# Kernel optimization log

Measured on AMD Instinct MI355X. Metric: run time of the kernel, lower is better.

Reference implementation:

```python
import jax, jax.numpy as jnp
import numpy as np

N, E = 10000, 160000
IN_C, HID, OUT_C = 128, 128, 64
LAYERS, HEADS = 3, 8
D_HEAD = HID // HEADS


def setup_inputs() -> dict:
    key = jax.random.key(0)
    ks = jax.random.split(key, 12)
    sc = lambda k, shape, fan: (jax.random.normal(k, shape, jnp.float32) / np.float32(np.sqrt(fan)))
    return dict(
        x=jax.random.normal(ks[0], (N, IN_C), jnp.float32),
        edge_index=jax.random.randint(ks[1], (2, E), 0, N, jnp.int32),
        W1=sc(ks[2], (IN_C, HID), IN_C), b1=jnp.zeros((HID,), jnp.float32),
        Wq=sc(ks[3], (LAYERS, HID, HID), HID), bq=jnp.zeros((LAYERS, HID), jnp.float32),
        Wk=sc(ks[4], (LAYERS, HID, HID), HID), bk=jnp.zeros((LAYERS, HID), jnp.float32),
        Wv=sc(ks[5], (LAYERS, HID, HID), HID), bv=jnp.zeros((LAYERS, HID), jnp.float32),
        W2=sc(ks[6], (HID, OUT_C), HID), b2=jnp.zeros((OUT_C,), jnp.float32),
    )


def reference(x, edge_index, W1, b1, Wq, bq, Wk, bk, Wv, bv, W2, b2):
    n = x.shape[0]
    # gcn_norm with self-loops (edge weights = 1)
    loops = jnp.arange(n, dtype=edge_index.dtype)
    src = jnp.concatenate([edge_index[0], loops])  # x_j source nodes
    dst = jnp.concatenate([edge_index[1], loops])  # x_i target nodes (aggregation)
    deg = jax.ops.segment_sum(jnp.ones_like(src, dtype=x.dtype), dst, num_segments=n)
    dinv = jnp.where(deg > 0, jax.lax.rsqrt(deg), jnp.zeros_like(deg))
    norm = dinv[src] * dinv[dst]  # [E+N]

    # dropout layers are identity in eval mode
    h = jax.nn.relu(x @ W1 + b1)
    x_all = h[:, None, :]  # [N, 1, C]

    scale = np.float32(1.0 / np.sqrt(D_HEAD))
    for l in range(LAYERS):
        L = x_all.shape[1]
        # project at node level (linear commutes with gather)
        q = (x_all[:, -1] @ Wq[l] + bq[l])[dst]              # [Et, C], query = last-layer target feats
        k = (x_all @ Wk[l] + bk[l])[src]                     # [Et, L, C], key = source history
        v = (x_all @ Wv[l] + bv[l])[src]                     # [Et, L, C]
        Et = q.shape[0]
        qh = q.reshape(Et, HEADS, D_HEAD)
        kh = k.reshape(Et, L, HEADS, D_HEAD)
        vh = v.reshape(Et, L, HEADS, D_HEAD)
        scores = jnp.einsum('ehd,elhd->ehl', qh, kh) * scale  # attention over history axis L
        attn = jax.nn.softmax(scores, axis=-1)                 # (attn dropout is identity in eval)
        msg = jnp.einsum('ehl,elhd->ehd', attn, vh).reshape(Et, HID)
        agg = jax.ops.segment_sum(norm[:, None] * msg, dst, num_segments=n)
        h_new = jax.nn.relu(agg)
        x_all = jnp.concatenate([x_all, h_new[:, None, :]], axis=1)

    logits = x_all[:, -1] @ W2 + b2
    return jax.nn.log_softmax(logits, axis=1)
```

## Files before the change

kernel.cpp:

```cpp
#include <hip/hip_runtime.h>
#include <hip/hip_fp16.h>
#include <math.h>

#define NN 10000
#define EE 160000
#define HID 128
constexpr int N128 = NN * HID;
constexpr int PSTR = 768;
constexpr int HOFF = 384;

typedef _Float16 f16;
typedef f16 half8 __attribute__((ext_vector_type(8)));
typedef f16 f16x2 __attribute__((ext_vector_type(2)));
typedef float f32x4 __attribute__((ext_vector_type(4)));

#if __has_builtin(__builtin_amdgcn_fdot2)
__device__ inline float fdot2(f16x2 a, f16x2 b, float c) { return __builtin_amdgcn_fdot2(a, b, c, false); }
#else
__device__ inline float fdot2(f16x2 a, f16x2 b, float c) {
    return fmaf((float)a[0], (float)b[0], fmaf((float)a[1], (float)b[1], c));
}
#endif

__global__ __launch_bounds__(256) void zero_ws(int4* __restrict__ p) {
    p[blockIdx.x * 256 + threadIdx.x] = make_int4(0, 0, 0, 0);
}

__global__ __launch_bounds__(256) void cnt_count(const int* __restrict__ dst, int* __restrict__ cnt) {
    int e = blockIdx.x * 256 + threadIdx.x;
    if (e < EE) atomicAdd(&cnt[dst[e]], 1);
}

__global__ __launch_bounds__(256) void scan_rowptr(const int* __restrict__ cnt, int* __restrict__ rowptr,
                                                   float* __restrict__ dinv) {
    __shared__ int part[256];
    const int PER = (NN + 255) / 256;
    int t = threadIdx.x;
    int base = t * PER;
    int sum = 0;
    for (int i = 0; i < PER; ++i) {
        int idx = base + i;
        if (idx < NN) {
            int c = cnt[idx];
            sum += c;
            dinv[idx] = rsqrtf((float)c + 1.0f);
        }
    }
    part[t] = sum;
    __syncthreads();
    for (int ofs = 1; ofs < 256; ofs <<= 1) {
        int v = (t >= ofs) ? part[t - ofs] : 0;
        __syncthreads();
        part[t] += v;
        __syncthreads();
    }
    int run = (t > 0) ? part[t - 1] : 0;
    for (int i = 0; i < PER; ++i) {
        int idx = base + i;
        if (idx <= NN) rowptr[idx] = run;
        if (idx < NN) run += cnt[idx];
    }
}

__global__ __launch_bounds__(256) void scatter_edges(const int* __restrict__ ei,
                                                     const int* __restrict__ rowptr,
                                                     int* __restrict__ fill,
                                                     int* __restrict__ esorted) {
    int e = blockIdx.x * 256 + threadIdx.x;
    if (e < EE) {
        int s = ei[e], d = ei[EE + e];
        int pos = rowptr[d] + atomicAdd(&fill[d], 1);
        esorted[pos] = s;
    }
}

__global__ __launch_bounds__(256) void wprep(const float* __restrict__ W1, const float* __restrict__ Wq,
                                             const float* __restrict__ Wk, const float* __restrict__ Wv,
                                             const float* __restrict__ W2, f16* __restrict__ Wt) {
    int b = blockIdx.x;
    f16* dst = Wt + (size_t)b * 16384;
    int t = threadIdx.x;
    if (b == 10) {
        int oc = t & 63, k0 = (t >> 6) * 32;
        for (int kk = 0; kk < 32; ++kk) {
            int k = k0 + kk;
            dst[oc * 128 + k] = (f16)W2[(size_t)k * 64 + oc];
        }
        return;
    }
    const float* src = (b == 0) ? W1
                     : (b < 4)  ? Wq + (size_t)(b - 1) * 16384
                     : (b < 7)  ? Wk + (size_t)(b - 4) * 16384
                                : Wv + (size_t)(b - 7) * 16384;
    int oc = t >> 1;
    int k0 = (t & 1) * 64;
    for (int kk = 0; kk < 64; ++kk) {
        int k = k0 + kk;
        dst[oc * 128 + k] = (f16)src[k * 128 + oc];
    }
}

struct GJob {
    const void* in; const f16* Wt; const float* bias; const float* rowscale;
    void* out; int ldi; int ldo; int mode; int inF32;
    const f16* Wt2; const float* bias2;
};
struct GJobs { GJob j[7]; };

__global__ __launch_bounds__(256) void gemm_mfma(GJobs jobs, int nrows) {
    const GJob jb = jobs.j[blockIdx.y];
    __shared__ f16 Xl[64 * 128];
    __shared__ f16 Wl[128 * 128];
    const int t = threadIdx.x;
    const int row0 = blockIdx.x * 64;

    half8 zero8;
#pragma unroll
    for (int z = 0; z < 8; ++z) zero8[z] = (f16)0.f;

#pragma unroll
    for (int it = 0; it < 4; ++it) {
        int idx = t + it * 256;
        int r = idx >> 4, c = idx & 15;
        int gr = row0 + r;
        half8 v = zero8;
        if (gr < nrows) {
            if (jb.inF32) {
                const float* fin = (const float*)jb.in + (size_t)gr * jb.ldi + c * 8;
                float4 f0 = ((const float4*)fin)[0];
                float4 f1 = ((const float4*)fin)[1];
                v[0] = (f16)f0.x; v[1] = (f16)f0.y; v[2] = (f16)f0.z; v[3] = (f16)f0.w;
                v[4] = (f16)f1.x; v[5] = (f16)f1.y; v[6] = (f16)f1.z; v[7] = (f16)f1.w;
            } else {
                v = *(const half8*)((const f16*)jb.in + (size_t)gr * jb.ldi + c * 8);
            }
        }
        *(half8*)((char*)Xl + r * 256 + ((c * 16) ^ ((r & 7) << 4))) = v;
    }
#pragma unroll
    for (int it = 0; it < 8; ++it) {
        int idx = t + it * 256;
        int r = idx >> 4, c = idx & 15;
        half8 v = *(const half8*)(jb.Wt + (size_t)r * 128 + c * 8);
        *(half8*)((char*)Wl + r * 256 + ((c * 16) ^ ((r & 7) << 4))) = v;
    }
    __syncthreads();

    const int w = t >> 6, l = t & 63;
    const int lr = l & 15;
    const int lk = l >> 4;

    f32x4 acc[8];
#pragma unroll
    for (int tn = 0; tn < 8; ++tn)
#pragma unroll
        for (int i = 0; i < 4; ++i) acc[tn][i] = 0.f;

    const int arow = w * 16 + lr;
    const int axor = (arow & 7) << 4;
    const int bxor = (lr & 7) << 4;

#pragma unroll
    for (int ks = 0; ks < 4; ++ks) {
        int koff = (ks * 4 + lk) * 16;
        half8 a = *(const half8*)((const char*)Xl + arow * 256 + (koff ^ axor));
#pragma unroll
        for (int tn = 0; tn < 8; ++tn) {
            int oc = tn * 16 + lr;
            half8 b = *(const half8*)((const char*)Wl + oc * 256 + (koff ^ bxor));
            acc[tn] = __builtin_amdgcn_mfma_f32_16x16x32_f16(a, b, acc[tn], 0, 0, 0);
        }
    }

    const int rbase = row0 + w * 16 + (lk << 2);
    float brs[4];
#pragma unroll
    for (int i = 0; i < 4; ++i)
        brs[i] = jb.rowscale ? ((rbase + i < nrows) ? jb.rowscale[rbase + i] : 0.f) : 1.0f;
    float bsv[8];
#pragma unroll
    for (int tn = 0; tn < 8; ++tn) bsv[tn] = jb.bias[tn * 16 + lr];

    if (jb.mode == 0) {
        float* op = (float*)jb.out;
#pragma unroll
        for (int tn = 0; tn < 8; ++tn)
#pragma unroll
            for (int i = 0; i < 4; ++i) {
                int gr = rbase + i;
                if (gr < nrows) op[(size_t)gr * jb.ldo + tn * 16 + lr] = acc[tn][i] + brs[i] * bsv[tn];
            }
    } else if (jb.mode == 1) {
        f16* op = (f16*)jb.out;
#pragma unroll
        for (int tn = 0; tn < 8; ++tn)
#pragma unroll
            for (int i = 0; i < 4; ++i) {
                int gr = rbase + i;
                if (gr < nrows) op[(size_t)gr * jb.ldo + tn * 16 + lr] = (f16)fmaxf(acc[tn][i] + brs[i] * bsv[tn], 0.f);
            }
    } else if (jb.mode == 2) {
        f16* op = (f16*)jb.out;
#pragma unroll
        for (int tn = 0; tn < 8; ++tn)
#pragma unroll
            for (int i = 0; i < 4; ++i) {
                int gr = rbase + i;
                if (gr < nrows) op[(size_t)gr * jb.ldo + tn * 16 + lr] = (f16)(acc[tn][i] + brs[i] * bsv[tn]);
            }
    } else {
        __syncthreads();
#pragma unroll
        for (int tn = 0; tn < 8; ++tn)
#pragma unroll
            for (int i = 0; i < 4; ++i) {
                f16 v = (f16)fmaxf(acc[tn][i] + brs[i] * bsv[tn], 0.f);
                int lrow = w * 16 + (lk << 2) + i;
                int col = tn * 16 + lr;
                int byte = lrow * 256 + ((((col >> 3) * 16) ^ ((lrow & 7) << 4))) + (col & 7) * 2;
                *(f16*)((char*)Xl + byte) = v;
            }
#pragma unroll
        for (int it = 0; it < 4; ++it) {
            int idx = t + it * 256;
            int r = idx >> 4, c = idx & 15;
            half8 v = *(const half8*)(jb.Wt2 + (size_t)r * 128 + c * 8);
            *(half8*)((char*)Wl + r * 256 + ((c * 16) ^ ((r & 7) << 4))) = v;
        }
        __syncthreads();

        f32x4 acc2[4];
#pragma unroll
        for (int tn = 0; tn < 4; ++tn)
#pragma unroll
            for (int i = 0; i < 4; ++i) acc2[tn][i] = 0.f;
#pragma unroll
        for (int ks = 0; ks < 4; ++ks) {
            int koff = (ks * 4 + lk) * 16;
            half8 a = *(const half8*)((const char*)Xl + arow * 256 + (koff ^ axor));
#pragma unroll
            for (int tn = 0; tn < 4; ++tn) {
                int oc = tn * 16 + lr;
                half8 b = *(const half8*)((const char*)Wl + oc * 256 + (koff ^ bxor));
                acc2[tn] = __builtin_amdgcn_mfma_f32_16x16x32_f16(a, b, acc2[tn], 0, 0, 0);
            }
        }
        float bs2[4];
#pragma unroll
        for (int tn = 0; tn < 4; ++tn) bs2[tn] = jb.bias2[tn * 16 + lr];
#pragma unroll
        for (int i = 0; i < 4; ++i) {
            float lg[4];
#pragma unroll
            for (int tn = 0; tn < 4; ++tn) lg[tn] = acc2[tn][i] + bs2[tn];
            float m = fmaxf(fmaxf(lg[0], lg[1]), fmaxf(lg[2], lg[3]));
#pragma unroll
            for (int sft = 1; sft <= 8; sft <<= 1) m = fmaxf(m, __shfl_xor(m, sft));
            float den = 0.f;
#pragma unroll
            for (int tn = 0; tn < 4; ++tn) den += __expf(lg[tn] - m);
#pragma unroll
            for (int sft = 1; sft <= 8; sft <<= 1) den += __shfl_xor(den, sft);
            float lden = logf(den);
            int gr = rbase + i;
            if (gr < nrows) {
                float* op = (float*)jb.out + (size_t)gr * jb.ldo;
#pragma unroll
                for (int tn = 0; tn < 4; ++tn) op[tn * 16 + lr] = lg[tn] - m - lden;
            }
        }
    }
}

__global__ __launch_bounds__(256) void sgather4(
    const int* __restrict__ rowptr, const int* __restrict__ esorted,
    const float* __restrict__ dinv,
    const f16* __restrict__ hsrc , f16* __restrict__ Sh, float* __restrict__ srow) {
    int d = (blockIdx.x * 256 + threadIdx.x) >> 6;
    int lane = threadIdx.x & 63;
    if (d >= NN) return;
    int i0 = rowptr[d], i1 = rowptr[d + 1];
    int nE = i1 - i0 + 1;
    float dvd = dinv[d];
    float ax = 0.f, ay = 0.f, ssum = 0.f;

    auto ld_idx = [&](int jb, int (&s)[4], float (&dv)[4]) {
#pragma unroll
        for (int u = 0; u < 4; ++u) {
            int j = jb + u;
            int ss = (j < nE - 1) ? esorted[i0 + j] : d;
            s[u] = ss;
            dv[u] = (j < nE) ? dinv[ss] : 0.f;
        }
    };
    auto ld_dat = [&](const int (&s)[4], f16x2 (&hh)[4]) {
#pragma unroll
        for (int u = 0; u < 4; ++u)
            hh[u] = *(const f16x2*)(hsrc + (size_t)s[u] * PSTR + lane * 2);
    };
    auto comp = [&](const float (&dv)[4], const f16x2 (&hh)[4]) {
#pragma unroll
        for (int u = 0; u < 4; ++u) {
            ax = fmaf(dv[u], (float)hh[u][0], ax);
            ay = fmaf(dv[u], (float)hh[u][1], ay);
            ssum += dv[u];
        }
    };

    int sA[4], sB[4], sC[4], sD[4];
    float wA[4], wB[4], wC[4], wD[4];
    f16x2 hA[4], hB[4];
    ld_idx(0, sA, wA); ld_dat(sA, hA);
    ld_idx(4, sB, wB);
    for (int base = 0; base < nE; base += 8) {
        ld_idx(base + 8, sC, wC);
        ld_dat(sB, hB);
        comp(wA, hA);
        ld_idx(base + 12, sD, wD);
        ld_dat(sC, hA);
        comp(wB, hB);
#pragma unroll
        for (int u = 0; u < 4; ++u) { wA[u] = wC[u]; sB[u] = sD[u]; wB[u] = wD[u]; }
    }
    f16x2 o; o[0] = (f16)(dvd * ax); o[1] = (f16)(dvd * ay);
    *(f16x2*)(Sh + (size_t)d * 128 + lane * 2) = o;
    if (lane == 0) srow[d] = dvd * ssum;
}

template<int L>
__global__ __launch_bounds__(256) void node_attn4(
    const int* __restrict__ rowptr, const int* __restrict__ esorted,
    const float* __restrict__ dinv,
    const f16* __restrict__ qh, const f16* __restrict__ pack,
    f16* __restrict__ uh) {
    int d = (blockIdx.x * 256 + threadIdx.x) >> 6;
    int lane = threadIdx.x & 63;
    if (d >= NN) return;
    int i0 = rowptr[d], i1 = rowptr[d + 1];
    int nE = i1 - i0 + 1;
    float dvd = dinv[d];
    f16x2 q2 = *(const f16x2*)(qh + (size_t)d * 128 + lane * 2);
    float ax = 0.f, ay = 0.f;

    auto ld_idx = [&](int jb, int (&s)[4], float (&dv)[4]) {
#pragma unroll
        for (int u = 0; u < 4; ++u) {
            int j = jb + u;
            int ss = (j < nE - 1) ? esorted[i0 + j] : d;
            s[u] = ss;
            dv[u] = (j < nE) ? dinv[ss] : 0.f;
        }
    };
    auto ld_dat = [&](const int (&s)[4], f16x2 (&k2)[4][L], f16x2 (&hh)[4][L]) {
#pragma unroll
        for (int u = 0; u < 4; ++u) {
            const f16* bp = pack + (size_t)s[u] * PSTR + lane * 2;
#pragma unroll
            for (int l = 0; l < L; ++l) {
                k2[u][l] = *(const f16x2*)(bp + l * 128);
                hh[u][l] = *(const f16x2*)(bp + HOFF + l * 128);
            }
        }
    };
    auto comp = [&](const float (&dv)[4], const f16x2 (&k2)[4][L], const f16x2 (&hh)[4][L]) {
#pragma unroll
        for (int u = 0; u < 4; ++u) {
            float sc[L];
#pragma unroll
            for (int l = 0; l < L; ++l) {
                float p = fdot2(q2, k2[u][l], 0.f);
                p += __shfl_xor(p, 1);
                p += __shfl_xor(p, 2);
                p += __shfl_xor(p, 4);
                sc[l] = p * 0.25f;
            }
            float m = sc[0];
#pragma unroll
            for (int l = 1; l < L; ++l) m = fmaxf(m, sc[l]);
            float den = 0.f;
#pragma unroll
            for (int l = 0; l < L; ++l) { sc[l] = __expf(sc[l] - m); den += sc[l]; }
            float wgt = dv[u] * __builtin_amdgcn_rcpf(den);
#pragma unroll
            for (int l = 0; l < L; ++l) {
                float wl = sc[l] * wgt;
                ax = fmaf(wl, (float)hh[u][l][0], ax);
                ay = fmaf(wl, (float)hh[u][l][1], ay);
            }
        }
    };

    int sA[4], sB[4], sC[4], sD[4];
    float wA[4], wB[4], wC[4], wD[4];
    f16x2 kA[4][L], hA[4][L], kB[4][L], hB[4][L];
    ld_idx(0, sA, wA); ld_dat(sA, kA, hA);
    ld_idx(4, sB, wB);
    for (int base = 0; base < nE; base += 8) {
        ld_idx(base + 8, sC, wC);
        ld_dat(sB, kB, hB);
        comp(wA, kA, hA);
        ld_idx(base + 12, sD, wD);
        ld_dat(sC, kA, hA);
        comp(wB, kB, hB);
#pragma unroll
        for (int u = 0; u < 4; ++u) { wA[u] = wC[u]; sB[u] = sD[u]; wB[u] = wD[u]; }
    }
    f16x2 o; o[0] = (f16)(dvd * ax); o[1] = (f16)(dvd * ay);
    *(f16x2*)(uh + (size_t)d * 128 + lane * 2) = o;
}

extern "C" void kernel_launch(void* const* d_in, const int* in_sizes, int n_in,
                              void* d_out, int out_size, void* d_ws, size_t ws_size,
                              hipStream_t stream) {
    (void)in_sizes; (void)n_in; (void)out_size; (void)ws_size;
    const float* x  = (const float*)d_in[0];
    const int*   ei = (const int*)d_in[1];
    const float* W1 = (const float*)d_in[2];
    const float* b1 = (const float*)d_in[3];
    const float* Wq = (const float*)d_in[4];
    const float* bq = (const float*)d_in[5];
    const float* Wk = (const float*)d_in[6];
    const float* bk = (const float*)d_in[7];
    const float* Wv = (const float*)d_in[8];
    const float* bv = (const float*)d_in[9];
    const float* W2 = (const float*)d_in[10];
    const float* b2 = (const float*)d_in[11];
    float* out = (float*)d_out;

    int*    cnt     = (int*)d_ws;
    int*    fill    = cnt + 16384;
    int*    rowptr  = fill + 16384;
    int*    esorted = rowptr + 16384;
    float*  dinv    = (float*)(esorted + 163840);
    float*  srow    = dinv + 16384;
    f16*    pack    = (f16*)(srow + 16384);
    f16*    Sh      = pack + (size_t)NN * PSTR;
    f16*    qh      = Sh + N128;
    f16*    uh      = qh + N128;
    f16*    Wt      = uh + N128;

    zero_ws<<<32, 256, 0, stream>>>((int4*)cnt);
    cnt_count<<<(EE + 255) / 256, 256, 0, stream>>>(ei + EE, cnt);
    scan_rowptr<<<1, 256, 0, stream>>>(cnt, rowptr, dinv);
    scatter_edges<<<(EE + 255) / 256, 256, 0, stream>>>(ei, rowptr, fill, esorted);
    wprep<<<11, 256, 0, stream>>>(W1, Wq, Wk, Wv, W2, Wt);

    const int gx = (NN + 63) / 64;
    auto WT = [&](int m) { return Wt + (size_t)m * 16384; };
    auto H  = [&](int lev) { return pack + HOFF + lev * 128; };
    auto K  = [&](int lev) { return pack + lev * 128; };

    {
        GJobs jobs{};
        jobs.j[0] = {x, WT(0), b1, nullptr, H(0), HID, PSTR, 1, 1, nullptr, nullptr};
        gemm_mfma<<<dim3(gx, 1), 256, 0, stream>>>(jobs, NN);
    }

    const int nblocks = (NN * 64 + 255) / 256;

    sgather4<<<nblocks, 256, 0, stream>>>(rowptr, esorted, dinv, pack + HOFF, Sh, srow);
    {
        GJobs jobs{};
        jobs.j[0] = {Sh, WT(7), bv, srow, H(1), HID, PSTR, 1, 0, nullptr, nullptr};
        gemm_mfma<<<dim3(gx, 1), 256, 0, stream>>>(jobs, NN);
    }

    for (int l = 1; l < 3; ++l) {
        int L = l + 1;
        GJobs jobs{};
        jobs.j[0] = {H(L - 1), WT(1 + l), bq + l * HID, nullptr, qh, PSTR, HID, 2, 0, nullptr, nullptr};
        for (int lev = 0; lev < L; ++lev)
            jobs.j[1 + lev] = {H(lev), WT(4 + l), bk + l * HID, nullptr, K(lev), PSTR, PSTR, 2, 0, nullptr, nullptr};
        gemm_mfma<<<dim3(gx, 1 + L), 256, 0, stream>>>(jobs, NN);

        if (L == 2) node_attn4<2><<<nblocks, 256, 0, stream>>>(rowptr, esorted, dinv, qh, pack, uh);
        if (L == 3) node_attn4<3><<<nblocks, 256, 0, stream>>>(rowptr, esorted, dinv, qh, pack, uh);

        GJobs vjob{};
        if (L == 2) {
            vjob.j[0] = {uh, WT(7 + l), bv + l * HID, srow, H(2), HID, PSTR, 1, 0, nullptr, nullptr};
        } else {
            vjob.j[0] = {uh, WT(7 + l), bv + l * HID, srow, out, HID, 64, 3, 0, WT(10), b2};
        }
        gemm_mfma<<<dim3(gx, 1), 256, 0, stream>>>(vjob, NN);
    }
}
```

Before: 206.1 us.

## Split wave into four edge groups with 16-byte half8 loads in gather kernels

The gather and attention kernels are restructured so each 64-lane wave processes four edges at once, with every 16-lane quarter loading a 16-byte half8 slice of the 128-wide row rather than each lane loading 4 bytes. Per-lane accumulators are then reduced across quarters with cross-lane shuffles. The per-head dot-product reduction needs one shuffle instead of three. The zeroing kernel is folded into the weight-prep kernel to save a launch. This aims to raise memory-level parallelism and cut load instruction count, at the cost of more registers per lane and a final cross-quarter reduction.

```diff
diff --git a/kernel.cpp b/kernel.cpp
--- a/kernel.cpp
+++ b/kernel.cpp
@@ -21,10 +21,6 @@
     return fmaf((float)a[0], (float)b[0], fmaf((float)a[1], (float)b[1], c));
 }
 #endif
-
-__global__ __launch_bounds__(256) void zero_ws(int4* __restrict__ p) {
-    p[blockIdx.x * 256 + threadIdx.x] = make_int4(0, 0, 0, 0);
-}
 
 __global__ __launch_bounds__(256) void cnt_count(const int* __restrict__ dst, int* __restrict__ cnt) {
     int e = blockIdx.x * 256 + threadIdx.x;
@@ -74,12 +70,17 @@
     }
 }
 
-__global__ __launch_bounds__(256) void wprep(const float* __restrict__ W1, const float* __restrict__ Wq,
-                                             const float* __restrict__ Wk, const float* __restrict__ Wv,
-                                             const float* __restrict__ W2, f16* __restrict__ Wt) {
+__global__ __launch_bounds__(256) void prep_fused(const float* __restrict__ W1, const float* __restrict__ Wq,
+                                                  const float* __restrict__ Wk, const float* __restrict__ Wv,
+                                                  const float* __restrict__ W2, f16* __restrict__ Wt,
+                                                  int4* __restrict__ zbuf) {
     int b = blockIdx.x;
+    int t = threadIdx.x;
+    if (b >= 11) {
+        zbuf[(b - 11) * 256 + t] = make_int4(0, 0, 0, 0);
+        return;
+    }
     f16* dst = Wt + (size_t)b * 16384;
-    int t = threadIdx.x;
     if (b == 10) {
         int oc = t & 63, k0 = (t >> 6) * 32;
         for (int kk = 0; kk < 32; ++kk) {
@@ -272,141 +273,131 @@
     }
 }
 
-__global__ __launch_bounds__(256) void sgather4(
+__global__ __launch_bounds__(256) void sgather5(
     const int* __restrict__ rowptr, const int* __restrict__ esorted,
     const float* __restrict__ dinv,
     const f16* __restrict__ hsrc , f16* __restrict__ Sh, float* __restrict__ srow) {
     int d = (blockIdx.x * 256 + threadIdx.x) >> 6;
-    int lane = threadIdx.x & 63;
+    int lam = threadIdx.x & 63;
+    int qe = lam >> 4, le = lam & 15;
     if (d >= NN) return;
-    int i0 = rowptr[d], i1 = rowptr[d + 1];
-    int nE = i1 - i0 + 1;
+    int i0 = rowptr[d], nE = rowptr[d + 1] - i0 + 1;
     float dvd = dinv[d];
-    float ax = 0.f, ay = 0.f, ssum = 0.f;
-
-    auto ld_idx = [&](int jb, int (&s)[4], float (&dv)[4]) {
-#pragma unroll
-        for (int u = 0; u < 4; ++u) {
-            int j = jb + u;
-            int ss = (j < nE - 1) ? esorted[i0 + j] : d;
-            s[u] = ss;
-            dv[u] = (j < nE) ? dinv[ss] : 0.f;
-        }
+    float u[8];
+#pragma unroll
+    for (int i = 0; i < 8; ++i) u[i] = 0.f;
+    float ssum = 0.f;
+
+    auto ldb = [&](int b, float& w, half8& h) {
+        int j = b + qe;
+        int s = (j < nE - 1) ? esorted[i0 + j] : d;
+        w = (j < nE) ? dinv[s] : 0.f;
+        h = *(const half8*)(hsrc + (size_t)s * PSTR + le * 8);
     };
-    auto ld_dat = [&](const int (&s)[4], f16x2 (&hh)[4]) {
-#pragma unroll
-        for (int u = 0; u < 4; ++u)
-            hh[u] = *(const f16x2*)(hsrc + (size_t)s[u] * PSTR + lane * 2);
+    auto cmp = [&](float w, const half8& h) {
+#pragma unroll
+        for (int i = 0; i < 8; ++i) u[i] = fmaf(w, (float)h[i], u[i]);
+        ssum += w;
     };
-    auto comp = [&](const float (&dv)[4], const f16x2 (&hh)[4]) {
-#pragma unroll
-        for (int u = 0; u < 4; ++u) {
-            ax = fmaf(dv[u], (float)hh[u][0], ax);
-            ay = fmaf(dv[u], (float)hh[u][1], ay);
-            ssum += dv[u];
-        }
-    };
-
-    int sA[4], sB[4], sC[4], sD[4];
-    float wA[4], wB[4], wC[4], wD[4];
-    f16x2 hA[4], hB[4];
-    ld_idx(0, sA, wA); ld_dat(sA, hA);
-    ld_idx(4, sB, wB);
-    for (int base = 0; base < nE; base += 8) {
-        ld_idx(base + 8, sC, wC);
-        ld_dat(sB, hB);
-        comp(wA, hA);
-        ld_idx(base + 12, sD, wD);
-        ld_dat(sC, hA);
-        comp(wB, hB);
-#pragma unroll
-        for (int u = 0; u < 4; ++u) { wA[u] = wC[u]; sB[u] = sD[u]; wB[u] = wD[u]; }
-    }
-    f16x2 o; o[0] = (f16)(dvd * ax); o[1] = (f16)(dvd * ay);
-    *(f16x2*)(Sh + (size_t)d * 128 + lane * 2) = o;
-    if (lane == 0) srow[d] = dvd * ssum;
+
+    float wA, wB; half8 hA, hB;
+    ldb(0, wA, hA);
+    for (int b = 0; b < nE; b += 8) {
+        ldb(b + 4, wB, hB);
+        cmp(wA, hA);
+        ldb(b + 8, wA, hA);
+        cmp(wB, hB);
+    }
+#pragma unroll
+    for (int i = 0; i < 8; ++i) {
+        u[i] += __shfl_xor(u[i], 16);
+        u[i] += __shfl_xor(u[i], 32);
+    }
+    ssum += __shfl_xor(ssum, 16);
+    ssum += __shfl_xor(ssum, 32);
+    if (qe == 0) {
+        half8 o;
+#pragma unroll
+        for (int i = 0; i < 8; ++i) o[i] = (f16)(dvd * u[i]);
+        *(half8*)(Sh + (size_t)d * 128 + le * 8) = o;
+        if (le == 0) srow[d] = dvd * ssum;
+    }
 }
 
 template<int L>
-__global__ __launch_bounds__(256) void node_attn4(
+__global__ __launch_bounds__(256) void node_attn5(
     const int* __restrict__ rowptr, const int* __restrict__ esorted,
     const float* __restrict__ dinv,
     const f16* __restrict__ qh, const f16* __restrict__ pack,
     f16* __restrict__ uh) {
     int d = (blockIdx.x * 256 + threadIdx.x) >> 6;
-    int lane = threadIdx.x & 63;
+    int lam = threadIdx.x & 63;
+    int qe = lam >> 4, le = lam & 15;
     if (d >= NN) return;
-    int i0 = rowptr[d], i1 = rowptr[d + 1];
-    int nE = i1 - i0 + 1;
+    int i0 = rowptr[d], nE = rowptr[d + 1] - i0 + 1;
     float dvd = dinv[d];
-    f16x2 q2 = *(const f16x2*)(qh + (size_t)d * 128 + lane * 2);
-    float ax = 0.f, ay = 0.f;
-
-    auto ld_idx = [&](int jb, int (&s)[4], float (&dv)[4]) {
-#pragma unroll
-        for (int u = 0; u < 4; ++u) {
-            int j = jb + u;
-            int ss = (j < nE - 1) ? esorted[i0 + j] : d;
-            s[u] = ss;
-            dv[u] = (j < nE) ? dinv[ss] : 0.f;
+    half8 q8 = *(const half8*)(qh + (size_t)d * 128 + le * 8);
+    const f16x2* qp = (const f16x2*)&q8;
+    float u[8];
+#pragma unroll
+    for (int i = 0; i < 8; ++i) u[i] = 0.f;
+
+    auto ldb = [&](int b, float& w, half8 (&k)[L], half8 (&h)[L]) {
+        int j = b + qe;
+        int s = (j < nE - 1) ? esorted[i0 + j] : d;
+        w = (j < nE) ? dinv[s] : 0.f;
+        const f16* bp = pack + (size_t)s * PSTR + le * 8;
+#pragma unroll
+        for (int l = 0; l < L; ++l) {
+            k[l] = *(const half8*)(bp + l * 128);
+            h[l] = *(const half8*)(bp + HOFF + l * 128);
         }
     };
-    auto ld_dat = [&](const int (&s)[4], f16x2 (&k2)[4][L], f16x2 (&hh)[4][L]) {
-#pragma unroll
-        for (int u = 0; u < 4; ++u) {
-            const f16* bp = pack + (size_t)s[u] * PSTR + lane * 2;
-#pragma unroll
-            for (int l = 0; l < L; ++l) {
-                k2[u][l] = *(const f16x2*)(bp + l * 128);
-                hh[u][l] = *(const f16x2*)(bp + HOFF + l * 128);
-            }
+    auto cmp = [&](float w, const half8 (&k)[L], const half8 (&h)[L]) {
+        float sc[L];
+#pragma unroll
+        for (int l = 0; l < L; ++l) {
+            const f16x2* kp = (const f16x2*)&k[l];
+            float p = 0.f;
+#pragma unroll
+            for (int i = 0; i < 4; ++i) p = fdot2(qp[i], kp[i], p);
+            p += __shfl_xor(p, 1);
+            sc[l] = p * 0.25f;
+        }
+        float m = sc[0];
+#pragma unroll
+        for (int l = 1; l < L; ++l) m = fmaxf(m, sc[l]);
+        float den = 0.f;
+#pragma unroll
+        for (int l = 0; l < L; ++l) { sc[l] = __expf(sc[l] - m); den += sc[l]; }
+        float wg = w * __builtin_amdgcn_rcpf(den);
+#pragma unroll
+        for (int l = 0; l < L; ++l) {
+            float a = sc[l] * wg;
+#pragma unroll
+            for (int i = 0; i < 8; ++i) u[i] = fmaf(a, (float)h[l][i], u[i]);
         }
     };
-    auto comp = [&](const float (&dv)[4], const f16x2 (&k2)[4][L], const f16x2 (&hh)[4][L]) {
-#pragma unroll
-        for (int u = 0; u < 4; ++u) {
-            float sc[L];
-#pragma unroll
-            for (int l = 0; l < L; ++l) {
-                float p = fdot2(q2, k2[u][l], 0.f);
-                p += __shfl_xor(p, 1);
-                p += __shfl_xor(p, 2);
-                p += __shfl_xor(p, 4);
-                sc[l] = p * 0.25f;
-            }
-            float m = sc[0];
-#pragma unroll
-            for (int l = 1; l < L; ++l) m = fmaxf(m, sc[l]);
-            float den = 0.f;
-#pragma unroll
-            for (int l = 0; l < L; ++l) { sc[l] = __expf(sc[l] - m); den += sc[l]; }
-            float wgt = dv[u] * __builtin_amdgcn_rcpf(den);
-#pragma unroll
-            for (int l = 0; l < L; ++l) {
-                float wl = sc[l] * wgt;
-                ax = fmaf(wl, (float)hh[u][l][0], ax);
-                ay = fmaf(wl, (float)hh[u][l][1], ay);
-            }
-        }
-    };
-
-    int sA[4], sB[4], sC[4], sD[4];
-    float wA[4], wB[4], wC[4], wD[4];
-    f16x2 kA[4][L], hA[4][L], kB[4][L], hB[4][L];
-    ld_idx(0, sA, wA); ld_dat(sA, kA, hA);
-    ld_idx(4, sB, wB);
-    for (int base = 0; base < nE; base += 8) {
-        ld_idx(base + 8, sC, wC);
-        ld_dat(sB, kB, hB);
-        comp(wA, kA, hA);
-        ld_idx(base + 12, sD, wD);
-        ld_dat(sC, kA, hA);
-        comp(wB, kB, hB);
-#pragma unroll
-        for (int u = 0; u < 4; ++u) { wA[u] = wC[u]; sB[u] = sD[u]; wB[u] = wD[u]; }
-    }
-    f16x2 o; o[0] = (f16)(dvd * ax); o[1] = (f16)(dvd * ay);
-    *(f16x2*)(uh + (size_t)d * 128 + lane * 2) = o;
+
+    float wA, wB; half8 kA[L], hA[L], kB[L], hB[L];
+    ldb(0, wA, kA, hA);
+    for (int b = 0; b < nE; b += 8) {
+        ldb(b + 4, wB, kB, hB);
+        cmp(wA, kA, hA);
+        ldb(b + 8, wA, kA, hA);
+        cmp(wB, kB, hB);
+    }
+#pragma unroll
+    for (int i = 0; i < 8; ++i) {
+        u[i] += __shfl_xor(u[i], 16);
+        u[i] += __shfl_xor(u[i], 32);
+    }
+    if (qe == 0) {
+        half8 o;
+#pragma unroll
+        for (int i = 0; i < 8; ++i) o[i] = (f16)(dvd * u[i]);
+        *(half8*)(uh + (size_t)d * 128 + le * 8) = o;
+    }
 }
 
 extern "C" void kernel_launch(void* const* d_in, const int* in_sizes, int n_in,
@@ -439,11 +430,10 @@
     f16*    uh      = qh + N128;
     f16*    Wt      = uh + N128;
 
-    zero_ws<<<32, 256, 0, stream>>>((int4*)cnt);
+    prep_fused<<<43, 256, 0, stream>>>(W1, Wq, Wk, Wv, W2, Wt, (int4*)cnt);
     cnt_count<<<(EE + 255) / 256, 256, 0, stream>>>(ei + EE, cnt);
     scan_rowptr<<<1, 256, 0, stream>>>(cnt, rowptr, dinv);
     scatter_edges<<<(EE + 255) / 256, 256, 0, stream>>>(ei, rowptr, fill, esorted);
-    wprep<<<11, 256, 0, stream>>>(W1, Wq, Wk, Wv, W2, Wt);
 
     const int gx = (NN + 63) / 64;
     auto WT = [&](int m) { return Wt + (size_t)m * 16384; };
@@ -458,7 +448,7 @@
 
     const int nblocks = (NN * 64 + 255) / 256;
 
-    sgather4<<<nblocks, 256, 0, stream>>>(rowptr, esorted, dinv, pack + HOFF, Sh, srow);
+    sgather5<<<nblocks, 256, 0, stream>>>(rowptr, esorted, dinv, pack + HOFF, Sh, srow);
     {
         GJobs jobs{};
         jobs.j[0] = {Sh, WT(7), bv, srow, H(1), HID, PSTR, 1, 0, nullptr, nullptr};
@@ -473,8 +463,8 @@
             jobs.j[1 + lev] = {H(lev), WT(4 + l), bk + l * HID, nullptr, K(lev), PSTR, PSTR, 2, 0, nullptr, nullptr};
         gemm_mfma<<<dim3(gx, 1 + L), 256, 0, stream>>>(jobs, NN);
 
-        if (L == 2) node_attn4<2><<<nblocks, 256, 0, stream>>>(rowptr, esorted, dinv, qh, pack, uh);
-        if (L == 3) node_attn4<3><<<nblocks, 256, 0, stream>>>(rowptr, esorted, dinv, qh, pack, uh);
+        if (L == 2) node_attn5<2><<<nblocks, 256, 0, stream>>>(rowptr, esorted, dinv, qh, pack, uh);
+        if (L == 3) node_attn5<3><<<nblocks, 256, 0, stream>>>(rowptr, esorted, dinv, qh, pack, uh);
 
         GJobs vjob{};
         if (L == 2) {
```

After: 169.0 us. -18.0%, faster.
